# Optimization experiments

Hardware: AMD Instinct MI355X
Metric: run time of the kernel (lower is better)

Reference implementation:

```python
import jax, jax.numpy as jnp
import numpy as np

S, B, IN, H, OUT, L = 512, 64, 512, 1024, 512, 2


def setup_inputs() -> dict:
    key = jax.random.key(0)
    ks = jax.random.split(key, 16)
    s = lambda k, *shape: jax.random.normal(k, shape, dtype=jnp.float32) * 0.02
    inp = {
        "x": jax.random.normal(ks[0], (S, B, IN), dtype=jnp.float32),
        "h0": jnp.zeros((L, B, H), dtype=jnp.float32),
        # layer 0 (input -> hidden)
        "Ua0": s(ks[1], IN, H), "Uc0": s(ks[2], IN, H), "Uh0": s(ks[3], IN, H),
        "wa0": jax.random.normal(ks[4], (H,), dtype=jnp.float32) * 0.02,
        "wc0": jax.random.normal(ks[5], (H,), dtype=jnp.float32) * 0.02,
        "ba0": jnp.zeros((H,), jnp.float32), "bc0": jnp.zeros((H,), jnp.float32), "bh0": jnp.zeros((H,), jnp.float32),
        # layer 1 (hidden -> hidden)
        "Ua1": s(ks[6], H, H), "Uc1": s(ks[7], H, H), "Uh1": s(ks[8], H, H),
        "wa1": jax.random.normal(ks[9], (H,), dtype=jnp.float32) * 0.02,
        "wc1": jax.random.normal(ks[10], (H,), dtype=jnp.float32) * 0.02,
        "ba1": jnp.zeros((H,), jnp.float32), "bc1": jnp.zeros((H,), jnp.float32), "bh1": jnp.zeros((H,), jnp.float32),
        # decoder
        "Wdec": s(ks[11], H, OUT), "bdec": jnp.zeros((OUT,), jnp.float32),
    }
    return inp


def _brc_layer(x, h0, Ua, Uc, Uh, wa, wc, ba, bc, bh):
    """Bistable Recurrent Cell layer over time-major x: [S, B, in] -> ([S,B,H], [B,H])."""
    # Precompute all input-to-hidden projections as one big GEMM each.
    xa = x @ Ua + ba  # [S,B,H]
    xc = x @ Uc + bc
    xh = x @ Uh + bh

    def step(h, xs):
        xa_t, xc_t, xh_t = xs
        a = 1.0 + jnp.tanh(xa_t + wa * h)
        c = jax.nn.sigmoid(xc_t + wc * h)
        h_new = c * h + (1.0 - c) * jnp.tanh(xh_t + a * h)
        return h_new, h_new

    h_last, ys = jax.lax.scan(step, h0, (xa, xc, xh))
    return ys, h_last


def reference(x, h0, Ua0, Uc0, Uh0, wa0, wc0, ba0, bc0, bh0,
              Ua1, Uc1, Uh1, wa1, wc1, ba1, bc1, bh1, Wdec, bdec):
    y0, h0_last = _brc_layer(x, h0[0], Ua0, Uc0, Uh0, wa0, wc0, ba0, bc0, bh0)
    # dropout = 0.0 -> identity between layers
    y1, h1_last = _brc_layer(y0, h0[1], Ua1, Uc1, Uh1, wa1, wc1, ba1, bc1, bh1)
    out = y1 @ Wdec + bdec  # sequential_output=True -> decode every timestep
    hidden = jnp.stack([h0_last, h1_last])  # [L, B, H]
    return out, hidden
```

## Files before the change

### kernel.cpp

```cpp
#include <hip/hip_runtime.h>
#include <math.h>

#define S_DIM 512
#define B_DIM 64
#define IN_DIM 512
#define H_DIM 1024
#define OUT_DIM 512
#define BH (B_DIM * H_DIM)

typedef unsigned short ushort_t;
typedef unsigned int uint_t;
using f32x4 = __attribute__((ext_vector_type(4))) float;
using f16x8 = __attribute__((ext_vector_type(8))) _Float16;

#define LO_SCALE 2048.0f
#define LO_INV   (1.0f / 2048.0f)

__device__ __forceinline__ void split_f16(float v, ushort_t& hi, ushort_t& lo) {
    _Float16 h = (_Float16)v;
    float r = (v - (float)h) * LO_SCALE;
    _Float16 l = (_Float16)r;
    hi = __builtin_bit_cast(ushort_t, h);
    lo = __builtin_bit_cast(ushort_t, l);
}

__device__ __forceinline__ float frcp(float x) { return __builtin_amdgcn_rcpf(x); }
__device__ __forceinline__ float fsig(float z) { return frcp(1.f + __expf(-z)); }
__device__ __forceinline__ float ftanh(float z) { return 1.f - 2.f * frcp(1.f + __expf(2.f * z)); }

__device__ __forceinline__ void gload_lds16(const ushort_t* g, ushort_t* l) {
    __builtin_amdgcn_global_load_lds(
        (const __attribute__((address_space(1))) void*)g,
        (__attribute__((address_space(3))) void*)l, 16, 0, 0);
}

__global__ __launch_bounds__(256) void transpose_split_f16(
    const float* __restrict__ W, ushort_t* __restrict__ Whi, ushort_t* __restrict__ Wlo,
    int K, int N)
{
    __shared__ float tile[32][33];
    const int k0 = blockIdx.y * 32, n0 = blockIdx.x * 32;
    const int tx = threadIdx.x & 31, ty = threadIdx.x >> 5;
#pragma unroll
    for (int r = 0; r < 32; r += 8)
        tile[ty + r][tx] = W[(size_t)(k0 + ty + r) * N + n0 + tx];
    __syncthreads();
#pragma unroll
    for (int r = 0; r < 32; r += 8) {
        ushort_t hi, lo;
        split_f16(tile[tx][ty + r], hi, lo);
        const size_t o = (size_t)(n0 + ty + r) * K + k0 + tx;
        Whi[o] = hi;
        Wlo[o] = lo;
    }
}

__global__ __launch_bounds__(256) void convert_split_f16(
    const float* __restrict__ src, ushort_t* __restrict__ dhi, ushort_t* __restrict__ dlo,
    int n)
{
    const int i = (blockIdx.x * 256 + threadIdx.x) * 4;
    if (i < n) {
        float4 v = *(const float4*)(src + i);
        ushort4 h, l;
        split_f16(v.x, h.x, l.x); split_f16(v.y, h.y, l.y);
        split_f16(v.z, h.z, l.z); split_f16(v.w, h.w, l.w);
        *(ushort4*)(dhi + i) = h;
        *(ushort4*)(dlo + i) = l;
    }
}

__global__ __launch_bounds__(256, 2) void mfma_gemm3_split(
    const ushort_t* __restrict__ Ahi, const ushort_t* __restrict__ Alo,
    const ushort_t* __restrict__ Wh0, const ushort_t* __restrict__ Wl0,
    const ushort_t* __restrict__ Wh1, const ushort_t* __restrict__ Wl1,
    const ushort_t* __restrict__ Wh2, const ushort_t* __restrict__ Wl2,
    const float* __restrict__ b0, const float* __restrict__ b1, const float* __restrict__ b2,
    float* __restrict__ C0, float* __restrict__ C1, float* __restrict__ C2,
    int M, int N, int K)
{
    const int NB = N >> 7;
    const int inner = blockIdx.x % (3 * NB);
    const int mb = blockIdx.x / (3 * NB);
    const int nb = inner % NB;
    const int z  = inner / NB;

    const ushort_t* __restrict__ Wh = (z == 0) ? Wh0 : (z == 1) ? Wh1 : Wh2;
    const ushort_t* __restrict__ Wl = (z == 0) ? Wl0 : (z == 1) ? Wl1 : Wl2;
    const float* __restrict__ bias  = (z == 0) ? b0  : (z == 1) ? b1  : b2;
    float* __restrict__ C           = (z == 0) ? C0  : (z == 1) ? C1  : C2;

    __shared__ __align__(16) ushort_t AsH[128 * 32];
    __shared__ __align__(16) ushort_t AsL[128 * 32];
    __shared__ __align__(16) ushort_t BsH[128 * 32];
    __shared__ __align__(16) ushort_t BsL[128 * 32];

    const int tid  = threadIdx.x;
    const int lane = tid & 63;
    const int wave = tid >> 6;
    const int quad = lane >> 4;
    const int l16  = lane & 15;
    const int wm   = wave >> 1;
    const int wn   = wave & 1;

    const int row0 = mb * 128;
    const int col0 = nb * 128;

    f32x4 accP[4][4] = {};
    f32x4 accQ[4][4] = {};

    for (int k0 = 0; k0 < K; k0 += 32) {
#pragma unroll
        for (int i = 0; i < 2; ++i) {
            const int c  = tid + i * 256;
            const int r  = c >> 2;
            const int kc = c & 3;
            const size_t ga = (size_t)(row0 + r) * K + k0 + kc * 8;
            const size_t gb = (size_t)(col0 + r) * K + k0 + kc * 8;
            gload_lds16(Ahi + ga, &AsH[c * 8]);
            gload_lds16(Alo + ga, &AsL[c * 8]);
            gload_lds16(Wh  + gb, &BsH[c * 8]);
            gload_lds16(Wl  + gb, &BsL[c * 8]);
        }
        __syncthreads();

        f16x8 ah[4], al[4], bh[4], bl[4];
#pragma unroll
        for (int i = 0; i < 4; ++i) {
            const int ro = (wm * 64 + i * 16 + l16) * 32 + quad * 8;
            ah[i] = *(const f16x8*)&AsH[ro];
            al[i] = *(const f16x8*)&AsL[ro];
        }
#pragma unroll
        for (int j = 0; j < 4; ++j) {
            const int ro = (wn * 64 + j * 16 + l16) * 32 + quad * 8;
            bh[j] = *(const f16x8*)&BsH[ro];
            bl[j] = *(const f16x8*)&BsL[ro];
        }

#pragma unroll
        for (int i = 0; i < 4; ++i)
#pragma unroll
            for (int j = 0; j < 4; ++j) {
                accP[i][j] = __builtin_amdgcn_mfma_f32_16x16x32_f16(ah[i], bh[j], accP[i][j], 0, 0, 0);
                accQ[i][j] = __builtin_amdgcn_mfma_f32_16x16x32_f16(ah[i], bl[j], accQ[i][j], 0, 0, 0);
                accQ[i][j] = __builtin_amdgcn_mfma_f32_16x16x32_f16(al[i], bh[j], accQ[i][j], 0, 0, 0);
            }
        __syncthreads();
    }

#pragma unroll
    for (int i = 0; i < 4; ++i) {
        const int row = row0 + wm * 64 + i * 16 + quad * 4;
#pragma unroll
        for (int j = 0; j < 4; ++j) {
            const int col = col0 + wn * 64 + j * 16 + l16;
            const float bv = bias[col];
#pragma unroll
            for (int r = 0; r < 4; ++r)
                C[(size_t)(row + r) * N + col] = accP[i][j][r] + accQ[i][j][r] * LO_INV + bv;
        }
    }
}

__global__ __launch_bounds__(256, 2) void mfma_gemm_dec(
    const ushort_t* __restrict__ A, const ushort_t* __restrict__ Wt,
    const float* __restrict__ bias, float* __restrict__ C,
    int M, int N, int K)
{
    const int NB = N >> 7;
    const int mb = blockIdx.x / NB;
    const int nb = blockIdx.x % NB;

    __shared__ __align__(16) ushort_t As[128 * 32];
    __shared__ __align__(16) ushort_t Bs[128 * 32];

    const int tid  = threadIdx.x;
    const int lane = tid & 63;
    const int wave = tid >> 6;
    const int quad = lane >> 4;
    const int l16  = lane & 15;
    const int wm   = wave >> 1;
    const int wn   = wave & 1;

    const int row0 = mb * 128;
    const int col0 = nb * 128;

    f32x4 acc[4][4] = {};

    for (int k0 = 0; k0 < K; k0 += 32) {
#pragma unroll
        for (int i = 0; i < 2; ++i) {
            const int c  = tid + i * 256;
            const int r  = c >> 2;
            const int kc = c & 3;
            gload_lds16(A  + (size_t)(row0 + r) * K + k0 + kc * 8, &As[c * 8]);
            gload_lds16(Wt + (size_t)(col0 + r) * K + k0 + kc * 8, &Bs[c * 8]);
        }
        __syncthreads();

        f16x8 af[4], bf[4];
#pragma unroll
        for (int i = 0; i < 4; ++i)
            af[i] = *(const f16x8*)&As[(wm * 64 + i * 16 + l16) * 32 + quad * 8];
#pragma unroll
        for (int j = 0; j < 4; ++j)
            bf[j] = *(const f16x8*)&Bs[(wn * 64 + j * 16 + l16) * 32 + quad * 8];

#pragma unroll
        for (int i = 0; i < 4; ++i)
#pragma unroll
            for (int j = 0; j < 4; ++j)
                acc[i][j] = __builtin_amdgcn_mfma_f32_16x16x32_f16(af[i], bf[j], acc[i][j], 0, 0, 0);
        __syncthreads();
    }

#pragma unroll
    for (int i = 0; i < 4; ++i) {
        const int row = row0 + wm * 64 + i * 16 + quad * 4;
#pragma unroll
        for (int j = 0; j < 4; ++j) {
            const int col = col0 + wn * 64 + j * 16 + l16;
            const float bv = bias[col];
#pragma unroll
            for (int r = 0; r < 4; ++r)
                C[(size_t)(row + r) * N + col] = acc[i][j][r] + bv;
        }
    }
}

template <bool WRITE_LO>
__global__ __launch_bounds__(256) void brc_scan_v3(
    const float* __restrict__ xa, const float* __restrict__ xc,
    const float* __restrict__ xh, const float* __restrict__ wa,
    const float* __restrict__ wc, const float* __restrict__ h_in,
    ushort_t* __restrict__ yhi, ushort_t* __restrict__ ylo,
    float* __restrict__ h_out, int T_c)
{
    const int idx = blockIdx.x * 256 + threadIdx.x;
    const int j = idx & (H_DIM - 1);
    float h = h_in[idx];
    const float waj = wa[j], wcj = wc[j];

    float pa[8], pc[8], ph[8];
#pragma unroll
    for (int d = 0; d < 8; ++d) {
        const int dd = (d < T_c) ? d : 0;
        const size_t b = (size_t)dd * BH + idx;
        pa[d] = xa[b]; pc[d] = xc[b]; ph[d] = xh[b];
    }

#pragma unroll 8
    for (int t = 0; t < T_c; ++t) {
        const int s = t & 7;
        const float ca = pa[s], cc = pc[s], ch = ph[s];
        const int tn = t + 8;
        if (tn < T_c) {
            const size_t b = (size_t)tn * BH + idx;
            pa[s] = xa[b]; pc[s] = xc[b]; ph[s] = xh[b];
        }
        const float a = 1.f + ftanh(ca + waj * h);
        const float c = fsig(cc + wcj * h);
        h = c * h + (1.f - c) * ftanh(ch + a * h);

        ushort_t hh, hl;
        split_f16(h, hh, hl);
        const size_t ob = (size_t)t * BH + idx;
        yhi[ob] = hh;
        if (WRITE_LO) ylo[ob] = hl;
    }
    h_out[idx] = h;
}

extern "C" void kernel_launch(void* const* d_in, const int* in_sizes, int n_in,
                              void* d_out, int out_size, void* d_ws, size_t ws_size,
                              hipStream_t stream) {
    const float* x    = (const float*)d_in[0];
    const float* h0   = (const float*)d_in[1];
    const float* Ua0  = (const float*)d_in[2];
    const float* Uc0  = (const float*)d_in[3];
    const float* Uh0  = (const float*)d_in[4];
    const float* wa0  = (const float*)d_in[5];
    const float* wc0  = (const float*)d_in[6];
    const float* ba0  = (const float*)d_in[7];
    const float* bc0  = (const float*)d_in[8];
    const float* bh0  = (const float*)d_in[9];
    const float* Ua1  = (const float*)d_in[10];
    const float* Uc1  = (const float*)d_in[11];
    const float* Uh1  = (const float*)d_in[12];
    const float* wa1  = (const float*)d_in[13];
    const float* wc1  = (const float*)d_in[14];
    const float* ba1  = (const float*)d_in[15];
    const float* bc1  = (const float*)d_in[16];
    const float* bh1  = (const float*)d_in[17];
    const float* Wdec = (const float*)d_in[18];
    const float* bdec = (const float*)d_in[19];

    float* outF = (float*)d_out;
    float* out_seq  = outF;
    float* h_last0  = outF + (size_t)S_DIM * B_DIM * OUT_DIM;
    float* h_last1  = h_last0 + BH;

    char* wsb = (char*)d_ws;
    size_t off = 0;
    auto alloc = [&](size_t bytes) -> void* {
        void* p = wsb + off;
        off += (bytes + 255) & ~(size_t)255;
        return p;
    };
    const size_t szL0 = (size_t)IN_DIM * H_DIM;
    const size_t szL1 = (size_t)H_DIM * H_DIM;
    const size_t szD  = (size_t)H_DIM * OUT_DIM;
    ushort_t *Wa0h = (ushort_t*)alloc(szL0 * 2), *Wa0l = (ushort_t*)alloc(szL0 * 2);
    ushort_t *Wc0h = (ushort_t*)alloc(szL0 * 2), *Wc0l = (ushort_t*)alloc(szL0 * 2);
    ushort_t *Wh0h = (ushort_t*)alloc(szL0 * 2), *Wh0l = (ushort_t*)alloc(szL0 * 2);
    ushort_t *Wa1h = (ushort_t*)alloc(szL1 * 2), *Wa1l = (ushort_t*)alloc(szL1 * 2);
    ushort_t *Wc1h = (ushort_t*)alloc(szL1 * 2), *Wc1l = (ushort_t*)alloc(szL1 * 2);
    ushort_t *Wh1h = (ushort_t*)alloc(szL1 * 2), *Wh1l = (ushort_t*)alloc(szL1 * 2);
    ushort_t *Wdh  = (ushort_t*)alloc(szD * 2),  *Wdl  = (ushort_t*)alloc(szD * 2);

    const size_t perT = (size_t)2 * B_DIM * IN_DIM * 2 + (size_t)3 * BH * 4 + (size_t)3 * BH * 2;
    int T_c = 512;
    while (T_c > 1 && off + (size_t)T_c * perT + 4096 > ws_size) T_c >>= 1;
    const size_t chunk_elems = (size_t)T_c * BH;
    const size_t xchunk_elems = (size_t)T_c * B_DIM * IN_DIM;

    ushort_t* xhib = (ushort_t*)alloc(xchunk_elems * 2);
    ushort_t* xlob = (ushort_t*)alloc(xchunk_elems * 2);
    float* g_a = (float*)alloc(chunk_elems * 4);
    float* g_c = (float*)alloc(chunk_elems * 4);
    float* g_h = (float*)alloc(chunk_elems * 4);
    ushort_t* y0h = (ushort_t*)alloc(chunk_elems * 2);
    ushort_t* y0l = (ushort_t*)alloc(chunk_elems * 2);
    ushort_t* y1h = (ushort_t*)alloc(chunk_elems * 2);

    const int n_chunks = S_DIM / T_c;
    const int Mc = T_c * B_DIM;

    transpose_split_f16<<<dim3(H_DIM / 32, IN_DIM / 32), 256, 0, stream>>>(Ua0, Wa0h, Wa0l, IN_DIM, H_DIM);
    transpose_split_f16<<<dim3(H_DIM / 32, IN_DIM / 32), 256, 0, stream>>>(Uc0, Wc0h, Wc0l, IN_DIM, H_DIM);
    transpose_split_f16<<<dim3(H_DIM / 32, IN_DIM / 32), 256, 0, stream>>>(Uh0, Wh0h, Wh0l, IN_DIM, H_DIM);
    transpose_split_f16<<<dim3(H_DIM / 32, H_DIM / 32), 256, 0, stream>>>(Ua1, Wa1h, Wa1l, H_DIM, H_DIM);
    transpose_split_f16<<<dim3(H_DIM / 32, H_DIM / 32), 256, 0, stream>>>(Uc1, Wc1h, Wc1l, H_DIM, H_DIM);
    transpose_split_f16<<<dim3(H_DIM / 32, H_DIM / 32), 256, 0, stream>>>(Uh1, Wh1h, Wh1l, H_DIM, H_DIM);
    transpose_split_f16<<<dim3(OUT_DIM / 32, H_DIM / 32), 256, 0, stream>>>(Wdec, Wdh, Wdl, H_DIM, OUT_DIM);

    dim3 blk(256);
    const int grid_g = (H_DIM / 128) * (Mc / 128) * 3;
    const int grid_d = (OUT_DIM / 128) * (Mc / 128);
    dim3 grid_scan(BH / 256);

    for (int ci = 0; ci < n_chunks; ++ci) {
        const float* x_chunk = x + (size_t)ci * Mc * IN_DIM;
        float* out_chunk = out_seq + (size_t)ci * Mc * OUT_DIM;

        convert_split_f16<<<dim3((int)(xchunk_elems / 4 / 256)), blk, 0, stream>>>(
            x_chunk, xhib, xlob, (int)xchunk_elems);

        mfma_gemm3_split<<<dim3(grid_g), blk, 0, stream>>>(
            xhib, xlob, Wa0h, Wa0l, Wc0h, Wc0l, Wh0h, Wh0l,
            ba0, bc0, bh0, g_a, g_c, g_h, Mc, H_DIM, IN_DIM);
        brc_scan_v3<true><<<grid_scan, blk, 0, stream>>>(
            g_a, g_c, g_h, wa0, wc0, (ci == 0) ? h0 : h_last0, y0h, y0l, h_last0, T_c);

        mfma_gemm3_split<<<dim3(grid_g), blk, 0, stream>>>(
            y0h, y0l, Wa1h, Wa1l, Wc1h, Wc1l, Wh1h, Wh1l,
            ba1, bc1, bh1, g_a, g_c, g_h, Mc, H_DIM, H_DIM);
        brc_scan_v3<false><<<grid_scan, blk, 0, stream>>>(
            g_a, g_c, g_h, wa1, wc1, (ci == 0) ? (h0 + BH) : h_last1, y1h, nullptr, h_last1, T_c);

        mfma_gemm_dec<<<dim3(grid_d), blk, 0, stream>>>(
            y1h, Wdh, bdec, out_chunk, Mc, OUT_DIM, H_DIM);
    }
}
```

Baseline: 1.641 ms.

## Double-buffer LDS tiles and XOR-swizzle K chunks in MFMA GEMMs

Both the split-precision projection GEMM and the decoder GEMM now use two LDS buffers. The next K-tile is issued before computing on the current one, which overlaps global loads with MFMA work and removes one barrier per iteration. The K-chunk placement in LDS is also XOR-swizzled by row, to reduce bank conflicts on the fragment reads. The cost is twice the LDS footprint (64KB for the split kernel), which may lower occupancy.

```diff
diff --git a/kernel.cpp b/kernel.cpp
--- a/kernel.cpp
+++ b/kernel.cpp
@@ -90,10 +90,10 @@
     const float* __restrict__ bias  = (z == 0) ? b0  : (z == 1) ? b1  : b2;
     float* __restrict__ C           = (z == 0) ? C0  : (z == 1) ? C1  : C2;
 
-    __shared__ __align__(16) ushort_t AsH[128 * 32];
-    __shared__ __align__(16) ushort_t AsL[128 * 32];
-    __shared__ __align__(16) ushort_t BsH[128 * 32];
-    __shared__ __align__(16) ushort_t BsL[128 * 32];
+    __shared__ __align__(16) ushort_t AsH[2][128 * 32];
+    __shared__ __align__(16) ushort_t AsL[2][128 * 32];
+    __shared__ __align__(16) ushort_t BsH[2][128 * 32];
+    __shared__ __align__(16) ushort_t BsL[2][128 * 32];
 
     const int tid  = threadIdx.x;
     const int lane = tid & 63;
@@ -109,33 +109,42 @@
     f32x4 accP[4][4] = {};
     f32x4 accQ[4][4] = {};
 
-    for (int k0 = 0; k0 < K; k0 += 32) {
+    auto STAGE = [&](int buf, int k0) {
 #pragma unroll
         for (int i = 0; i < 2; ++i) {
             const int c  = tid + i * 256;
             const int r  = c >> 2;
-            const int kc = c & 3;
+            const int kc = (c & 3) ^ ((r >> 1) & 3);
             const size_t ga = (size_t)(row0 + r) * K + k0 + kc * 8;
             const size_t gb = (size_t)(col0 + r) * K + k0 + kc * 8;
-            gload_lds16(Ahi + ga, &AsH[c * 8]);
-            gload_lds16(Alo + ga, &AsL[c * 8]);
-            gload_lds16(Wh  + gb, &BsH[c * 8]);
-            gload_lds16(Wl  + gb, &BsL[c * 8]);
-        }
+            gload_lds16(Ahi + ga, &AsH[buf][c * 8]);
+            gload_lds16(Alo + ga, &AsL[buf][c * 8]);
+            gload_lds16(Wh  + gb, &BsH[buf][c * 8]);
+            gload_lds16(Wl  + gb, &BsL[buf][c * 8]);
+        }
+    };
+
+    const int nt = K >> 5;
+    STAGE(0, 0);
+    int cur = 0;
+    const int gq = (quad ^ ((l16 >> 1) & 3)) * 8;
+
+    for (int t = 0; t < nt; ++t) {
         __syncthreads();
+        if (t + 1 < nt) STAGE(cur ^ 1, (t + 1) << 5);
 
         f16x8 ah[4], al[4], bh[4], bl[4];
 #pragma unroll
         for (int i = 0; i < 4; ++i) {
-            const int ro = (wm * 64 + i * 16 + l16) * 32 + quad * 8;
-            ah[i] = *(const f16x8*)&AsH[ro];
-            al[i] = *(const f16x8*)&AsL[ro];
+            const int ro = (wm * 64 + i * 16 + l16) * 32 + gq;
+            ah[i] = *(const f16x8*)&AsH[cur][ro];
+            al[i] = *(const f16x8*)&AsL[cur][ro];
         }
 #pragma unroll
         for (int j = 0; j < 4; ++j) {
-            const int ro = (wn * 64 + j * 16 + l16) * 32 + quad * 8;
-            bh[j] = *(const f16x8*)&BsH[ro];
-            bl[j] = *(const f16x8*)&BsL[ro];
+            const int ro = (wn * 64 + j * 16 + l16) * 32 + gq;
+            bh[j] = *(const f16x8*)&BsH[cur][ro];
+            bl[j] = *(const f16x8*)&BsL[cur][ro];
         }
 
 #pragma unroll
@@ -146,7 +155,7 @@
                 accQ[i][j] = __builtin_amdgcn_mfma_f32_16x16x32_f16(ah[i], bl[j], accQ[i][j], 0, 0, 0);
                 accQ[i][j] = __builtin_amdgcn_mfma_f32_16x16x32_f16(al[i], bh[j], accQ[i][j], 0, 0, 0);
             }
-        __syncthreads();
+        cur ^= 1;
     }
 
 #pragma unroll
@@ -172,8 +181,8 @@
     const int mb = blockIdx.x / NB;
     const int nb = blockIdx.x % NB;
 
-    __shared__ __align__(16) ushort_t As[128 * 32];
-    __shared__ __align__(16) ushort_t Bs[128 * 32];
+    __shared__ __align__(16) ushort_t As[2][128 * 32];
+    __shared__ __align__(16) ushort_t Bs[2][128 * 32];
 
     const int tid  = threadIdx.x;
     const int lane = tid & 63;
@@ -188,31 +197,40 @@
 
     f32x4 acc[4][4] = {};
 
-    for (int k0 = 0; k0 < K; k0 += 32) {
+    auto STAGE = [&](int buf, int k0) {
 #pragma unroll
         for (int i = 0; i < 2; ++i) {
             const int c  = tid + i * 256;
             const int r  = c >> 2;
-            const int kc = c & 3;
-            gload_lds16(A  + (size_t)(row0 + r) * K + k0 + kc * 8, &As[c * 8]);
-            gload_lds16(Wt + (size_t)(col0 + r) * K + k0 + kc * 8, &Bs[c * 8]);
-        }
+            const int kc = (c & 3) ^ ((r >> 1) & 3);
+            gload_lds16(A  + (size_t)(row0 + r) * K + k0 + kc * 8, &As[buf][c * 8]);
+            gload_lds16(Wt + (size_t)(col0 + r) * K + k0 + kc * 8, &Bs[buf][c * 8]);
+        }
+    };
+
+    const int nt = K >> 5;
+    STAGE(0, 0);
+    int cur = 0;
+    const int gq = (quad ^ ((l16 >> 1) & 3)) * 8;
+
+    for (int t = 0; t < nt; ++t) {
         __syncthreads();
+        if (t + 1 < nt) STAGE(cur ^ 1, (t + 1) << 5);
 
         f16x8 af[4], bf[4];
 #pragma unroll
         for (int i = 0; i < 4; ++i)
-            af[i] = *(const f16x8*)&As[(wm * 64 + i * 16 + l16) * 32 + quad * 8];
+            af[i] = *(const f16x8*)&As[cur][(wm * 64 + i * 16 + l16) * 32 + gq];
 #pragma unroll
         for (int j = 0; j < 4; ++j)
-            bf[j] = *(const f16x8*)&Bs[(wn * 64 + j * 16 + l16) * 32 + quad * 8];
+            bf[j] = *(const f16x8*)&Bs[cur][(wn * 64 + j * 16 + l16) * 32 + gq];
 
 #pragma unroll
         for (int i = 0; i < 4; ++i)
 #pragma unroll
             for (int j = 0; j < 4; ++j)
                 acc[i][j] = __builtin_amdgcn_mfma_f32_16x16x32_f16(af[i], bf[j], acc[i][j], 0, 0, 0);
-        __syncthreads();
+        cur ^= 1;
     }
 
 #pragma unroll
```

Result: no change. 1.664 ms (+1.4%).
